# Performance work log

Measured on AMD Instinct MI355X. Metric: run time of the kernel, lower is better.

The kernel has to match this reference:

```python
import jax, jax.numpy as jnp
import numpy as np
from jax.scipy.special import ndtr, logsumexp

N_STATES = 64
DIM = 16
BATCH = 256
L = 16
_A_np, _B_np = np.nonzero(np.triu(np.ones((N_STATES, N_STATES))))  # pair indices, C = K(K+1)/2
N_CAT = len(_A_np)  # 2080
A_IDX = jnp.asarray(_A_np, dtype=jnp.int32)
B_IDX = jnp.asarray(_B_np, dtype=jnp.int32)


def setup_inputs() -> dict:
    key = jax.random.key(0)
    k1, k2, k3 = jax.random.split(key, 3)
    z = jax.random.normal(k1, (BATCH, L, DIM), dtype=jnp.float32)
    mu = jax.random.uniform(k2, (DIM, N_STATES), minval=-1.0, maxval=1.0, dtype=jnp.float32)
    log_pi = jax.random.normal(k3, (1, N_CAT), dtype=jnp.float32) * 0.1
    return {"z": z, "mu": mu, "log_pi": log_pi}


def reference(z, mu, log_pi):
    # Training path of LatentSpace.call (inference=False) -> scalar log_p_z
    eps = 1e-16
    dt = z.dtype
    log2pi = jnp.log(jnp.asarray(2.0 * np.pi, dt))

    mu_B = mu[:, B_IDX]                     # [d, C]
    alpha = mu_B - mu[:, A_IDX]             # [d, C]  (mu_B - mu_A)
    beta = z[..., None] - mu_B[None, None]  # [B, L, d, C]

    inv_sig = jnp.sum(alpha * alpha, axis=0)                 # [C]
    safe = jnp.where(inv_sig == 0, jnp.asarray(1.0, dt), inv_sig)
    recip = jnp.where(inv_sig == 0, jnp.asarray(0.0, dt), 1.0 / safe)  # reciprocal_no_nan

    nu = -jnp.einsum('dc,bldc->blc', alpha, beta) * recip    # [B, L, C]
    bb = jnp.sum(beta * beta, axis=2)                        # [B, L, C]
    t = -bb + nu ** 2 * inv_sig

    cl = jnp.clip(inv_sig, 1e-12, 1e30)
    log_eta0 = 0.5 * (log2pi - jnp.log(cl) + t)
    sq = jnp.sqrt(cl)
    eta1 = (1.0 - nu) * sq
    eta2 = -nu * sq

    log_p_z_c_L = log_eta0 + jnp.log(jnp.clip(ndtr(eta1) - ndtr(eta2), eps, 1e30))

    temp_pi = jnp.clip(jax.nn.softmax(log_pi, axis=-1), eps, 1.0)[:, None, :]  # [1,1,C]
    log_p_zc_L = (-0.5 * DIM * log2pi + jnp.log(temp_pi)
                  + jnp.where(inv_sig == 0, -0.5 * bb, log_p_z_c_L))           # [B,L,C]
    log_p_z_L = logsumexp(log_p_zc_L, axis=-1, keepdims=True)                  # [B,L,1]
    return jnp.mean(log_p_z_L)
```

## Files before the change

kernel.cpp:

```cpp
#include <hip/hip_runtime.h>
#include <math.h>

#define N_STATES 64
#define DIM 16
#define N_CAT 2080
#define N_CAT_PAD 2304
#define N_ROWS 4096
#define N_ITER 9
#define LOG2PI 1.8378770664093453f
#define SQRT1_2 0.70710678118654752f
#define LN2 0.69314718055994531f


__device__ __forceinline__ float erfc_fast(float x) {
    const float ax = fabsf(x);
    const float t = __builtin_amdgcn_rcpf(fmaf(0.5f, ax, 1.0f));
    float p = 0.17087277f;
    p = fmaf(t, p, -0.82215223f);
    p = fmaf(t, p,  1.48851587f);
    p = fmaf(t, p, -1.13520398f);
    p = fmaf(t, p,  0.27886807f);
    p = fmaf(t, p, -0.18628806f);
    p = fmaf(t, p,  0.09678418f);
    p = fmaf(t, p,  0.37409196f);
    p = fmaf(t, p,  1.00002368f);
    p = fmaf(t, p, -1.26551223f);
    const float w = fmaf(-ax, ax, p);
    const float r = t * __expf(w);
    return (x < 0.0f) ? (2.0f - r) : r;
}

__global__ __launch_bounds__(256) void precompute_kernel(
        const float* __restrict__ mu,
        const float* __restrict__ log_pi,
        float* __restrict__ ws) {
    const int c = blockIdx.x * 256 + threadIdx.x;
    if (c >= N_CAT_PAD) return;

    float4* tab4 = (float4*)ws;
    float2* tab2 = (float2*)(ws + N_CAT_PAD * 4);

    if (c >= N_CAT) {
        tab4[c] = make_float4(0.f, -1e4f, 0.f, 0.f);
        float2 t2; t2.x = __int_as_float(0); t2.y = 60.f;
        tab2[c] = t2;
        return;
    }

    int a = (int)((129.0 - sqrt(129.0 * 129.0 - 8.0 * (double)c)) * 0.5);
    a = max(0, min(63, a));
    while (a > 0  && (64 * a - a * (a - 1) / 2) > c) a--;
    while (a < 63 && (64 * (a + 1) - (a + 1) * a / 2) <= c) a++;
    const int b = a + (c - (64 * a - a * (a - 1) / 2));

    float inv = 0.f, K = 0.f, m2b = 0.f;
    for (int d = 0; d < DIM; ++d) {
        const float ma = mu[d * N_STATES + a];
        const float mb = mu[d * N_STATES + b];
        const float al = mb - ma;
        inv += al * al;
        K   += al * mb;
        m2b += mb * mb;
    }
    const float cl   = fminf(fmaxf(inv, 1e-12f), 1e30f);
    const float lp   = log_pi[c];
    const float sq2  = sqrtf(cl) * SQRT1_2;
    const bool  diag = (a == b);
    const float rcp  = diag ? 0.f : 1.f / inv;

    float c0p = lp - 0.5f * m2b;
    c0p += diag ? LN2 : 0.5f * (LOG2PI - logf(cl));

    tab4[c] = make_float4(K, c0p, 0.5f * rcp, -rcp * sq2);
    float2 t2; t2.x = __int_as_float(a | (b << 16)); t2.y = diag ? 60.f : sq2;
    tab2[c] = t2;
}

__global__ __launch_bounds__(256) void row_kernel(
        const float* __restrict__ z,
        const float* __restrict__ mu,
        const float* __restrict__ ws,
        float* __restrict__ rows) {
    const int row = blockIdx.x;
    const int tid = threadIdx.x;
    __shared__ float zdot[N_STATES];
    __shared__ float zz_sh;
    __shared__ float wsum[4];

    const float* zr = z + row * DIM;
    if (tid < 64) {
        float acc = 0.f;
        #pragma unroll
        for (int d = 0; d < DIM; ++d) acc += zr[d] * mu[d * N_STATES + tid];
        zdot[tid] = acc;
    } else if (tid == 64) {
        float acc = 0.f;
        #pragma unroll
        for (int d = 0; d < DIM; ++d) acc += zr[d] * zr[d];
        zz_sh = acc;
    }
    __syncthreads();

    const float4* tab4 = (const float4*)ws;
    const float2* tab2 = (const float2*)(ws + N_CAT_PAD * 4);

    float s = 0.f;
    #pragma unroll
    for (int i = 0; i < N_ITER; ++i) {
        const int c = tid + i * 256;
        const float4 t4 = tab4[c];
        const float2 t2 = tab2[c];
        const int ab = __float_as_int(t2.x);
        const float sa = zdot[ab & 0xffff];
        const float sb = zdot[ab >> 16];
        const float dot = (sb - sa) - t4.x;
        const float y2 = dot * t4.w;
        const float y1 = y2 - t2.y;
        const float k  = fmaf(dot * t4.z, dot, t4.y + sb);
        float diff = 0.5f * (erfc_fast(y1) - erfc_fast(y2));
        diff = fminf(fmaxf(diff, 1e-16f), 1e30f);
        s = fmaf(diff, __expf(k), s);
    }

    #pragma unroll
    for (int off = 32; off > 0; off >>= 1)
        s += __shfl_xor(s, off);
    const int wave = tid >> 6;
    if ((tid & 63) == 0) wsum[wave] = s;
    __syncthreads();
    if (tid == 0) {
        const float S = (wsum[0] + wsum[1]) + (wsum[2] + wsum[3]);
        rows[row] = logf(S) - 0.5f * zz_sh;
    }
}

__global__ __launch_bounds__(256) void final_kernel(
        const float* __restrict__ rows,
        const float* __restrict__ log_pi,
        float* __restrict__ out) {
    __shared__ float red[256];
    const int tid = threadIdx.x;

    float mx = -INFINITY;
    for (int c = tid; c < N_CAT; c += 256) mx = fmaxf(mx, log_pi[c]);
    red[tid] = mx; __syncthreads();
    for (int off = 128; off > 0; off >>= 1) {
        if (tid < off) red[tid] = fmaxf(red[tid], red[tid + off]);
        __syncthreads();
    }
    const float gmax = red[0]; __syncthreads();
    float sm = 0.f;
    for (int c = tid; c < N_CAT; c += 256) sm += __expf(log_pi[c] - gmax);
    red[tid] = sm; __syncthreads();
    for (int off = 128; off > 0; off >>= 1) {
        if (tid < off) red[tid] += red[tid + off];
        __syncthreads();
    }
    const float lse = gmax + logf(red[0]); __syncthreads();

    float s = 0.f;
    for (int i = tid; i < N_ROWS; i += 256) s += rows[i];
    red[tid] = s; __syncthreads();
    for (int off = 128; off > 0; off >>= 1) {
        if (tid < off) red[tid] += red[tid + off];
        __syncthreads();
    }
    if (tid == 0)
        out[0] = red[0] * (1.0f / N_ROWS) - lse - 8.0f * LOG2PI;
}

extern "C" void kernel_launch(void* const* d_in, const int* in_sizes, int n_in,
                              void* d_out, int out_size, void* d_ws, size_t ws_size,
                              hipStream_t stream) {
    const float* z      = (const float*)d_in[0];
    const float* mu     = (const float*)d_in[1];
    const float* log_pi = (const float*)d_in[2];
    float* ws   = (float*)d_ws;
    float* rows = ws + N_CAT_PAD * 6;

    precompute_kernel<<<N_CAT_PAD / 256, 256, 0, stream>>>(mu, log_pi, ws);
    row_kernel<<<N_ROWS, 256, 0, stream>>>(z, mu, ws, rows);
    final_kernel<<<1, 256, 0, stream>>>(rows, log_pi, (float*)d_out);
}
```

Measured before the change: 83.13 us.

## Process two rows per block and fuse final reduction via last-block atomic

Each row block now handles two rows, so every category table load is reused for both rows, and the padded tail iteration is replaced by a 32-thread tail. The separate final kernel is removed: a global atomic counter lets the last finishing block compute the log_pi logsumexp and the mean over rows, which saves one launch. The clamp is reduced to a max with zero. Risks are the serial tail work in one block, higher register pressure from computing two rows per thread, and a behaviour change in the clamp (a difference of exactly zero now gives log(0) contributions only through the sum).

```diff
diff --git a/kernel.cpp b/kernel.cpp
--- a/kernel.cpp
+++ b/kernel.cpp
@@ -6,7 +6,10 @@
 #define N_CAT 2080
 #define N_CAT_PAD 2304
 #define N_ROWS 4096
-#define N_ITER 9
+#define ROWS_PER_BLOCK 2
+#define GRID_ROWS (N_ROWS / ROWS_PER_BLOCK)
+#define N_FULL_ITER 8
+#define N_TAIL 32
 #define LOG2PI 1.8378770664093453f
 #define SQRT1_2 0.70710678118654752f
 #define LN2 0.69314718055994531f
@@ -35,17 +38,9 @@
         const float* __restrict__ log_pi,
         float* __restrict__ ws) {
     const int c = blockIdx.x * 256 + threadIdx.x;
-    if (c >= N_CAT_PAD) return;
-
-    float4* tab4 = (float4*)ws;
-    float2* tab2 = (float2*)(ws + N_CAT_PAD * 4);
-
-    if (c >= N_CAT) {
-        tab4[c] = make_float4(0.f, -1e4f, 0.f, 0.f);
-        float2 t2; t2.x = __int_as_float(0); t2.y = 60.f;
-        tab2[c] = t2;
-        return;
-    }
+    if (blockIdx.x == 0 && threadIdx.x == 0)
+        *(int*)(ws + N_CAT_PAD * 6 + N_ROWS) = 0;
+    if (c >= N_CAT) return;
 
     int a = (int)((129.0 - sqrt(129.0 * 129.0 - 8.0 * (double)c)) * 0.5);
     a = max(0, min(63, a));
@@ -71,6 +66,8 @@
     float c0p = lp - 0.5f * m2b;
     c0p += diag ? LN2 : 0.5f * (LOG2PI - logf(cl));
 
+    float4* tab4 = (float4*)ws;
+    float2* tab2 = (float2*)(ws + N_CAT_PAD * 4);
     tab4[c] = make_float4(K, c0p, 0.5f * rcp, -rcp * sq2);
     float2 t2; t2.x = __int_as_float(a | (b << 16)); t2.y = diag ? 60.f : sq2;
     tab2[c] = t2;
@@ -79,67 +76,93 @@
 __global__ __launch_bounds__(256) void row_kernel(
         const float* __restrict__ z,
         const float* __restrict__ mu,
-        const float* __restrict__ ws,
-        float* __restrict__ rows) {
-    const int row = blockIdx.x;
+        const float* __restrict__ log_pi,
+        float* __restrict__ ws,
+        float* __restrict__ out) {
+    const int blk = blockIdx.x;
     const int tid = threadIdx.x;
-    __shared__ float zdot[N_STATES];
-    __shared__ float zz_sh;
-    __shared__ float wsum[4];
-
-    const float* zr = z + row * DIM;
-    if (tid < 64) {
+    __shared__ float zdot[ROWS_PER_BLOCK][N_STATES];
+    __shared__ float zz_sh[ROWS_PER_BLOCK];
+    __shared__ float wred[2][4];
+    __shared__ int   last_sh;
+    __shared__ float red[256];
+
+    const float* zr = z + (blk * ROWS_PER_BLOCK) * DIM;
+    if (tid < 128) {
+        const int r = tid >> 6, st = tid & 63;
         float acc = 0.f;
         #pragma unroll
-        for (int d = 0; d < DIM; ++d) acc += zr[d] * mu[d * N_STATES + tid];
-        zdot[tid] = acc;
-    } else if (tid == 64) {
+        for (int d = 0; d < DIM; ++d) acc += zr[r * DIM + d] * mu[d * N_STATES + st];
+        zdot[r][st] = acc;
+    } else if (tid < 128 + ROWS_PER_BLOCK) {
+        const int r = tid - 128;
         float acc = 0.f;
         #pragma unroll
-        for (int d = 0; d < DIM; ++d) acc += zr[d] * zr[d];
-        zz_sh = acc;
+        for (int d = 0; d < DIM; ++d) acc += zr[r * DIM + d] * zr[r * DIM + d];
+        zz_sh[r] = acc;
     }
     __syncthreads();
 
     const float4* tab4 = (const float4*)ws;
     const float2* tab2 = (const float2*)(ws + N_CAT_PAD * 4);
 
-    float s = 0.f;
-    #pragma unroll
-    for (int i = 0; i < N_ITER; ++i) {
-        const int c = tid + i * 256;
+    float s0 = 0.f, s1 = 0.f;
+
+    auto body = [&](int c) {
         const float4 t4 = tab4[c];
         const float2 t2 = tab2[c];
         const int ab = __float_as_int(t2.x);
-        const float sa = zdot[ab & 0xffff];
-        const float sb = zdot[ab >> 16];
-        const float dot = (sb - sa) - t4.x;
-        const float y2 = dot * t4.w;
-        const float y1 = y2 - t2.y;
-        const float k  = fmaf(dot * t4.z, dot, t4.y + sb);
-        float diff = 0.5f * (erfc_fast(y1) - erfc_fast(y2));
-        diff = fminf(fmaxf(diff, 1e-16f), 1e30f);
-        s = fmaf(diff, __expf(k), s);
-    }
+        const int ia = ab & 0xffff;
+        const int ib = ab >> 16;
+        {
+            const float sa = zdot[0][ia], sb = zdot[0][ib];
+            const float dot = (sb - sa) - t4.x;
+            const float y2 = dot * t4.w;
+            const float y1 = y2 - t2.y;
+            const float k  = fmaf(dot * t4.z, dot, t4.y + sb);
+            const float diff = fmaxf(0.5f * (erfc_fast(y1) - erfc_fast(y2)), 0.f);
+            s0 = fmaf(diff, __expf(k), s0);
+        }
+        {
+            const float sa = zdot[1][ia], sb = zdot[1][ib];
+            const float dot = (sb - sa) - t4.x;
+            const float y2 = dot * t4.w;
+            const float y1 = y2 - t2.y;
+            const float k  = fmaf(dot * t4.z, dot, t4.y + sb);
+            const float diff = fmaxf(0.5f * (erfc_fast(y1) - erfc_fast(y2)), 0.f);
+            s1 = fmaf(diff, __expf(k), s1);
+        }
+    };
 
     #pragma unroll
-    for (int off = 32; off > 0; off >>= 1)
-        s += __shfl_xor(s, off);
+    for (int i = 0; i < N_FULL_ITER; ++i) body(tid + i * 256);
+    if (tid < N_TAIL) body(2048 + tid);
+
+    #pragma unroll
+    for (int off = 32; off > 0; off >>= 1) {
+        s0 += __shfl_xor(s0, off);
+        s1 += __shfl_xor(s1, off);
+    }
     const int wave = tid >> 6;
-    if ((tid & 63) == 0) wsum[wave] = s;
+    if ((tid & 63) == 0) { wred[0][wave] = s0; wred[1][wave] = s1; }
     __syncthreads();
+
+    float* rows    = ws + N_CAT_PAD * 6;
+    int*   counter = (int*)(ws + N_CAT_PAD * 6 + N_ROWS);
     if (tid == 0) {
-        const float S = (wsum[0] + wsum[1]) + (wsum[2] + wsum[3]);
-        rows[row] = logf(S) - 0.5f * zz_sh;
-    }
-}
-
-__global__ __launch_bounds__(256) void final_kernel(
-        const float* __restrict__ rows,
-        const float* __restrict__ log_pi,
-        float* __restrict__ out) {
-    __shared__ float red[256];
-    const int tid = threadIdx.x;
+        const float S0 = (wred[0][0] + wred[0][1]) + (wred[0][2] + wred[0][3]);
+        const float S1 = (wred[1][0] + wred[1][1]) + (wred[1][2] + wred[1][3]);
+        rows[blk * 2 + 0] = logf(S0) - 0.5f * zz_sh[0];
+        rows[blk * 2 + 1] = logf(S1) - 0.5f * zz_sh[1];
+        __threadfence();
+        const int t = __hip_atomic_fetch_add(counter, 1, __ATOMIC_ACQ_REL,
+                                             __HIP_MEMORY_SCOPE_AGENT);
+        last_sh = (t == GRID_ROWS - 1);
+    }
+    __syncthreads();
+    if (!last_sh) return;
+
+    __threadfence();
 
     float mx = -INFINITY;
     for (int c = tid; c < N_CAT; c += 256) mx = fmaxf(mx, log_pi[c]);
@@ -159,7 +182,8 @@
     const float lse = gmax + logf(red[0]); __syncthreads();
 
     float s = 0.f;
-    for (int i = tid; i < N_ROWS; i += 256) s += rows[i];
+    for (int i = tid; i < N_ROWS; i += 256)
+        s += __hip_atomic_load(&rows[i], __ATOMIC_RELAXED, __HIP_MEMORY_SCOPE_AGENT);
     red[tid] = s; __syncthreads();
     for (int off = 128; off > 0; off >>= 1) {
         if (tid < off) red[tid] += red[tid + off];
@@ -175,10 +199,8 @@
     const float* z      = (const float*)d_in[0];
     const float* mu     = (const float*)d_in[1];
     const float* log_pi = (const float*)d_in[2];
-    float* ws   = (float*)d_ws;
-    float* rows = ws + N_CAT_PAD * 6;
-
-    precompute_kernel<<<N_CAT_PAD / 256, 256, 0, stream>>>(mu, log_pi, ws);
-    row_kernel<<<N_ROWS, 256, 0, stream>>>(z, mu, ws, rows);
-    final_kernel<<<1, 256, 0, stream>>>(rows, log_pi, (float*)d_out);
-}
+    float* ws = (float*)d_ws;
+
+    precompute_kernel<<<(N_CAT + 255) / 256, 256, 0, stream>>>(mu, log_pi, ws);
+    row_kernel<<<GRID_ROWS, 256, 0, stream>>>(z, mu, log_pi, ws, (float*)d_out);
+}
```

New measurement: 139.0 us. 67.2% more time.
